# Kernel optimization log

Hardware: AMD Instinct MI355X
Metric: run time of the kernel (lower is better)

Reference implementation:

```python
import jax, jax.numpy as jnp
import numpy as np

NEG_INF = -1e38


def wkv(k, v, w, u):
    """Log-sum-exp-stabilized RWKV WKV scan.
    k, v: (B, T, C); w, u: (C,). Returns y: (B, T, C).
    """
    B, T, C = k.shape

    def step(carry, kv_t):
        num, den, mx = carry            # each (B, C)
        k_t, v_t = kv_t                 # (B, C)
        ku = k_t + u
        m = jnp.maximum(mx, ku)
        e1 = jnp.exp(mx - m)
        e2 = jnp.exp(ku - m)
        y = (e1 * num + e2 * v_t) / (e1 * den + e2)
        # state update
        mw = mx + w
        m2 = jnp.maximum(mw, k_t)
        es1 = jnp.exp(mw - m2)
        es2 = jnp.exp(k_t - m2)
        num = es1 * num + es2 * v_t
        den = es1 * den + es2
        return (num, den, m2), y

    init = (jnp.zeros((B, C), k.dtype),
            jnp.zeros((B, C), k.dtype),
            jnp.full((B, C), NEG_INF, k.dtype))
    _, y = jax.lax.scan(step, init, (jnp.swapaxes(k, 0, 1), jnp.swapaxes(v, 0, 1)))
    return jnp.swapaxes(y, 0, 1)


def setup_inputs() -> dict:
    key = jax.random.key(0)
    ks = jax.random.split(key, 8)
    B, T, C = 8, 4096, 512
    x = jax.random.normal(ks[0], (B, T, C), dtype=jnp.float32)
    # Linear weights stored as (in, out) so forward is x @ W.
    W_rkv = jax.random.normal(ks[1], (C, 6 * C), dtype=jnp.float32) / np.sqrt(C)
    W_out = jax.random.normal(ks[2], (2 * C, C), dtype=jnp.float32) / np.sqrt(2 * C)
    time_decay = jax.random.uniform(ks[3], (C,), minval=-6.0, maxval=-5.0, dtype=jnp.float32)
    time_first = jax.random.uniform(ks[4], (C,), minval=-3.0, maxval=0.0, dtype=jnp.float32)
    time_decay_rev = jax.random.uniform(ks[5], (C,), minval=-6.0, maxval=-5.0, dtype=jnp.float32)
    time_first_rev = jax.random.uniform(ks[6], (C,), minval=-3.0, maxval=0.0, dtype=jnp.float32)
    return {"x": x, "W_rkv": W_rkv, "W_out": W_out,
            "time_decay": time_decay, "time_first": time_first,
            "time_decay_rev": time_decay_rev, "time_first_rev": time_first_rev}


def reference(x, W_rkv, W_out, time_decay, time_first, time_decay_rev, time_first_rev):
    B, T, C = x.shape
    rkv = (x @ W_rkv).reshape(B, T, 2, 3, C)
    # forward direction
    r_f, k_f, v_f = rkv[:, :, 0, 0], rkv[:, :, 0, 1], rkv[:, :, 0, 2]
    w_f = -jnp.exp(time_decay)
    out_f = jax.nn.sigmoid(r_f) * wkv(k_f, v_f, w_f, time_first)
    # backward direction (run scan on time-reversed k/v, then reverse back)
    r_b, k_b, v_b = rkv[:, :, 1, 0], rkv[:, :, 1, 1], rkv[:, :, 1, 2]
    w_b = -jnp.exp(time_decay_rev)
    out_b = wkv(k_b[:, ::-1], v_b[:, ::-1], w_b, time_first_rev)[:, ::-1]
    out_b = jax.nn.sigmoid(r_b) * out_b
    out_cat = jnp.concatenate([out_f, out_b], axis=-1)  # (B, T, 2C)
    return out_cat @ W_out
```

## Files before the change

### kernel.cpp

```cpp
#include <hip/hip_runtime.h>

typedef float f4 __attribute__((ext_vector_type(4)));
typedef unsigned short us4 __attribute__((ext_vector_type(4)));
typedef unsigned short us8 __attribute__((ext_vector_type(8)));
typedef __bf16 bf16x8 __attribute__((ext_vector_type(8)));
typedef float f32x4 __attribute__((ext_vector_type(4)));
typedef _Float16 h8 __attribute__((ext_vector_type(8)));

#define TT 4096
#define CCH 512
#define NCH2 256
#define CHL2 16
#define NSEG 32
#define SEGC 8

__device__ __forceinline__ unsigned short f2bf(float f) {
  unsigned u = __builtin_bit_cast(unsigned, f);
  unsigned r = (u + 0x7FFFu + ((u >> 16) & 1u)) >> 16;
  return (unsigned short)r;
}
__device__ __forceinline__ void gload_lds16(const void* g, void* l) {
  __builtin_amdgcn_global_load_lds(
      (const __attribute__((address_space(1))) unsigned int*)g,
      (__attribute__((address_space(3))) unsigned int*)l, 16, 0, 0);
}
#define VMCNT(n) asm volatile("s_waitcnt vmcnt(" #n ")" ::: "memory")

__global__ __launch_bounds__(256)
void convert_f32_bf16(const float* __restrict__ in, unsigned short* __restrict__ out, int n4) {
  int i = blockIdx.x * 256 + threadIdx.x;
  if (i >= n4) return;
  f4 f = *(const f4*)(in + (size_t)i * 4);
  us4 o = { f2bf(f[0]), f2bf(f[1]), f2bf(f[2]), f2bf(f[3]) };
  *(us4*)(out + (size_t)i * 4) = o;
}

__global__ __launch_bounds__(256)
void transpose_to_bf16(const float* __restrict__ in, unsigned short* __restrict__ out,
                       int R, int Cc) {
  __shared__ unsigned short tile[32][33];
  int c0 = blockIdx.x * 32, r0 = blockIdx.y * 32;
  int tx = threadIdx.x, ty = threadIdx.y;
  #pragma unroll
  for (int j = 0; j < 32; j += 8)
    tile[ty + j][tx] = f2bf(in[(size_t)(r0 + ty + j) * Cc + c0 + tx]);
  __syncthreads();
  #pragma unroll
  for (int j = 0; j < 32; j += 8)
    out[(size_t)(c0 + ty + j) * R + r0 + tx] = tile[tx][ty + j];
}

__global__ __launch_bounds__(512, 2)
void gemm256_g1(const unsigned short* __restrict__ A,
                const unsigned short* __restrict__ BT,
                _Float16* __restrict__ kbuf, _Float16* __restrict__ vbuf,
                _Float16* __restrict__ rbuf) {
  __shared__ char lds[131072];
  const int tid = threadIdx.x;
  const int lane = tid & 63, wv = tid >> 6;
  const int wm = wv >> 2, wn = wv & 3;
  const int ln15 = lane & 15, lq = lane >> 4;

  const int nwg = gridDim.x;
  const int bid = blockIdx.x;
  const int wgid = (nwg % 8 == 0) ? (bid % 8) * (nwg / 8) + bid / 8 : bid;
  const int bn = wgid % 12, bm = wgid / 12;
  const size_t m0 = (size_t)bm * 256, n0 = (size_t)bn * 256;
  const char* Ab = (const char*)(A + m0 * 512);
  const char* Bb = (const char*)(BT + n0 * 512);

  const int srow0 = tid >> 2, srow1 = 128 + (tid >> 2);
  const int sg = tid & 3;
  const int sgs0 = (sg ^ ((srow0 >> 1) & 3)) << 4;
  const int sgs1 = (sg ^ ((srow1 >> 1) & 3)) << 4;

  auto STAGE = [&](int mat, int t, int h) {
    const char* gsrc = mat ? Bb : Ab;
    char* ldst = lds + mat * 65536 + ((t & 1) << 15) + (h << 14);
    const size_t co = (size_t)t * 128 + (size_t)h * 64;
    gload_lds16(gsrc + (size_t)srow0 * 1024 + co + sgs0, ldst + tid * 16);
    gload_lds16(gsrc + (size_t)srow1 * 1024 + co + sgs1, ldst + 8192 + tid * 16);
  };

  f32x4 acc[8][4] = {};
  STAGE(0, 0, 0); STAGE(1, 0, 0); STAGE(0, 0, 1); STAGE(1, 0, 1);

  for (int t = 0; t < 8; ++t) {
    char* Abase = lds + ((t & 1) << 15);
    char* Bbase = lds + 65536 + ((t & 1) << 15);
    VMCNT(4);
    __builtin_amdgcn_s_barrier();
    __builtin_amdgcn_sched_barrier(0);
    {
      bf16x8 bf[4], af[8];
      #pragma unroll
      for (int fn = 0; fn < 4; ++fn) {
        const int r = wn * 64 + fn * 16 + ln15;
        bf[fn] = *(const bf16x8*)(Bbase + r * 64 + ((lq ^ ((r >> 1) & 3)) << 4));
      }
      #pragma unroll
      for (int fm = 0; fm < 8; ++fm) {
        const int r = wm * 128 + fm * 16 + ln15;
        af[fm] = *(const bf16x8*)(Abase + r * 64 + ((lq ^ ((r >> 1) & 3)) << 4));
      }
      if (t < 7) { STAGE(0, t + 1, 0); STAGE(1, t + 1, 0); }
      __builtin_amdgcn_s_setprio(1);
      #pragma unroll
      for (int fm = 0; fm < 8; ++fm)
        #pragma unroll
        for (int fn = 0; fn < 4; ++fn)
          acc[fm][fn] = __builtin_amdgcn_mfma_f32_16x16x32_bf16(af[fm], bf[fn], acc[fm][fn], 0, 0, 0);
      __builtin_amdgcn_s_setprio(0);
    }
    if (t < 7) { VMCNT(4); } else { VMCNT(0); }
    __builtin_amdgcn_s_barrier();
    __builtin_amdgcn_sched_barrier(0);
    {
      bf16x8 bf[4], af[8];
      #pragma unroll
      for (int fn = 0; fn < 4; ++fn) {
        const int r = wn * 64 + fn * 16 + ln15;
        bf[fn] = *(const bf16x8*)(Bbase + 16384 + r * 64 + ((lq ^ ((r >> 1) & 3)) << 4));
      }
      #pragma unroll
      for (int fm = 0; fm < 8; ++fm) {
        const int r = wm * 128 + fm * 16 + ln15;
        af[fm] = *(const bf16x8*)(Abase + 16384 + r * 64 + ((lq ^ ((r >> 1) & 3)) << 4));
      }
      if (t < 7) { STAGE(0, t + 1, 1); STAGE(1, t + 1, 1); }
      __builtin_amdgcn_s_setprio(1);
      #pragma unroll
      for (int fm = 0; fm < 8; ++fm)
        #pragma unroll
        for (int fn = 0; fn < 4; ++fn)
          acc[fm][fn] = __builtin_amdgcn_mfma_f32_16x16x32_bf16(af[fm], bf[fn], acc[fm][fn], 0, 0, 0);
      __builtin_amdgcn_s_setprio(0);
    }
  }

  const int n0i = (int)n0;
  const int dir = (n0i >= 1536) ? 1 : 0;
  const int jj0 = n0i - dir * 1536;
  const int seg = jj0 >> 9;
  const int cbase = jj0 & 511;
  _Float16* dbuf = (seg == 0) ? rbuf : (seg == 1 ? kbuf : vbuf);
  float* stg = (float*)lds;
  const int ebnd = wv >> 2;
  const int erow = (tid >> 3) & 31;
  const int el8 = tid & 7;
  __syncthreads();
  #pragma unroll
  for (int gi = 0; gi < 4; ++gi) {
    #pragma unroll
    for (int f2 = 0; f2 < 2; ++f2) {
      const int fm = gi * 2 + f2;
      #pragma unroll
      for (int q = 0; q < 4; ++q) {
        const int rloc = f2 * 16 + lq * 4 + q;
        float* dst = stg + wm * 8192 + rloc * 256;
        const int sw = ((rloc >> 2) & 1) << 4;
        #pragma unroll
        for (int fn = 0; fn < 4; ++fn)
          dst[(wn * 64 + fn * 16 + ln15) ^ sw] = acc[fm][fn][q];
      }
    }
    __syncthreads();
    {
      const int rowg = (int)m0 + ebnd * 128 + gi * 32 + erow;
      const int b_ = rowg >> 12, tt = rowg & 4095;
      const int trow = dir ? (4095 - tt) : tt;
      _Float16* gp = dbuf + ((size_t)(b_ * 2 + dir) * TT + trow) * 512 + cbase;
      const float* sp = stg + ebnd * 8192 + erow * 256;
      const int sw = ((erow >> 2) & 1) << 4;
      #pragma unroll
      for (int u = 0; u < 4; ++u) {
        const int cf = el8 * 8 + u * 64;
        const int cs = cf ^ sw;
        f4 a = *(const f4*)(sp + cs);
        f4 b = *(const f4*)(sp + cs + 4);
        h8 hv = { (_Float16)a[0], (_Float16)a[1], (_Float16)a[2], (_Float16)a[3],
                  (_Float16)b[0], (_Float16)b[1], (_Float16)b[2], (_Float16)b[3] };
        *(h8*)(gp + cf) = hv;
      }
    }
    __syncthreads();
  }
}

__global__ __launch_bounds__(256)
void gemm_bf16_m1(const unsigned short* __restrict__ A, int lda,
                  const unsigned short* __restrict__ BT, int ldb,
                  int M, int N, int K, float* __restrict__ out) {
  __shared__ char smem[16384];
  unsigned short* As  = (unsigned short*)smem;
  unsigned short* Bsm = (unsigned short*)(smem + 8192);
  const int tid = threadIdx.x;
  const int lane = tid & 63, wv = tid >> 6;
  const int wr = wv >> 1, wc = wv & 1;
  const int ln15 = lane & 15, lq = lane >> 4;
  const int mtiles = M >> 7;
  const int bm = blockIdx.x % mtiles, bn = blockIdx.x / mtiles;
  const size_t m0 = (size_t)bm << 7, n0 = (size_t)bn << 7;
  f32x4 acc[4][4] = {};
  const char* Ab = (const char*)(A + m0 * (size_t)lda);
  const char* Bb = (const char*)(BT + n0 * (size_t)ldb);
  const int r0 = tid >> 2;
  const int cb = (((tid & 3) ^ (r0 & 3)) << 4);
  const size_t ldab = (size_t)lda * 2, ldbb = (size_t)ldb * 2;

  for (int k0 = 0; k0 < K; k0 += 32) {
    const size_t kb = (size_t)k0 * 2;
    gload_lds16(Ab + (size_t)r0 * ldab + kb + cb,        (char*)As + tid * 16);
    gload_lds16(Ab + (size_t)(r0 + 64) * ldab + kb + cb, (char*)As + 4096 + tid * 16);
    gload_lds16(Bb + (size_t)r0 * ldbb + kb + cb,        (char*)Bsm + tid * 16);
    gload_lds16(Bb + (size_t)(r0 + 64) * ldbb + kb + cb, (char*)Bsm + 4096 + tid * 16);
    __syncthreads();
    bf16x8 af[4], bg[4];
    #pragma unroll
    for (int i = 0; i < 4; ++i) {
      const int ar = wr * 64 + i * 16 + ln15;
      const int br = wc * 64 + i * 16 + ln15;
      af[i] = *(const bf16x8*)((char*)As  + ((ar * 4 + (lq ^ (ar & 3))) << 4));
      bg[i] = *(const bf16x8*)((char*)Bsm + ((br * 4 + (lq ^ (br & 3))) << 4));
    }
    #pragma unroll
    for (int i = 0; i < 4; ++i)
      #pragma unroll
      for (int j = 0; j < 4; ++j)
        acc[i][j] = __builtin_amdgcn_mfma_f32_16x16x32_bf16(af[i], bg[j], acc[i][j], 0, 0, 0);
    __syncthreads();
  }

  const int tq = tid >> 3, t8 = tid & 7;
  #pragma unroll
  for (int i = 0; i < 4; ++i) {
    __syncthreads();
    float* st = (float*)smem;
    #pragma unroll
    for (int j = 0; j < 4; ++j) {
      const int cl = wc * 64 + j * 16 + ln15;
      #pragma unroll
      for (int q = 0; q < 4; ++q) {
        const int rl = wr * 16 + lq * 4 + q;
        st[rl * 128 + (cl ^ (((rl >> 2) & 3) << 4))] = acc[i][j][q];
      }
    }
    __syncthreads();
    const int rl = tq, lqp = (rl >> 2) & 3;
    const int lr = ((rl >> 4) << 6) + (i << 4) + (rl & 15);
    const int rowg = (int)m0 + lr;
    #pragma unroll
    for (int u = 0; u < 4; ++u) {
      const int colL = t8 * 16 + u * 4;
      const int colS = colL ^ (lqp << 4);
      f4 vv = *(const f4*)(st + rl * 128 + colS);
      *(f4*)(out + (size_t)rowg * N + n0 + colL) = vv;
    }
  }
}

__global__ __launch_bounds__(128)
void wkv_pass1(const _Float16* __restrict__ kbuf, const _Float16* __restrict__ vbuf,
               const float* __restrict__ td, const float* __restrict__ tdr,
               float* __restrict__ cN, float* __restrict__ cD, float* __restrict__ cM) {
  const int bd = blockIdx.x;
  const int ch = blockIdx.y * 2 + threadIdx.y;
  const int dir = bd & 1;
  const int c = threadIdx.x * 8;
  const float* tdp = (dir ? tdr : td) + c;
  float w[8], num[8], den[8], m[8];
  #pragma unroll
  for (int e = 0; e < 8; ++e) { w[e] = -__expf(tdp[e]); num[e] = 0.f; den[e] = 0.f; m[e] = -1e38f; }
  const size_t base = ((size_t)bd * TT + (size_t)ch * CHL2) * CCH + c;
  const _Float16* kp = kbuf + base;
  const _Float16* vp = vbuf + base;
  h8 ka = *(const h8*)(kp), va = *(const h8*)(vp);
  h8 kb = *(const h8*)(kp + CCH), vb = *(const h8*)(vp + CCH);
  for (int t = 0; t < CHL2; ++t) {
    h8 kc = {}, vc = {};
    if (t + 2 < CHL2) {
      kc = *(const h8*)(kp + (size_t)(t + 2) * CCH);
      vc = *(const h8*)(vp + (size_t)(t + 2) * CCH);
    }
    #pragma unroll
    for (int e = 0; e < 8; ++e) {
      float ke = (float)ka[e], ve = (float)va[e];
      float mw = m[e] + w[e];
      float m2 = fmaxf(mw, ke);
      float e1 = __expf(mw - m2), e2 = __expf(ke - m2);
      num[e] = e1 * num[e] + e2 * ve;
      den[e] = e1 * den[e] + e2;
      m[e] = m2;
    }
    ka = kb; va = vb; kb = kc; vb = vc;
  }
  const size_t ci = ((size_t)bd * NCH2 + ch) * CCH + c;
  #pragma unroll
  for (int h = 0; h < 2; ++h) {
    *(f4*)(cN + ci + h * 4) = (f4){num[h*4], num[h*4+1], num[h*4+2], num[h*4+3]};
    *(f4*)(cD + ci + h * 4) = (f4){den[h*4], den[h*4+1], den[h*4+2], den[h*4+3]};
    *(f4*)(cM + ci + h * 4) = (f4){m[h*4], m[h*4+1], m[h*4+2], m[h*4+3]};
  }
}

__global__ __launch_bounds__(128)
void wkv_p2a(const float* __restrict__ td, const float* __restrict__ tdr,
             const float* __restrict__ cN, const float* __restrict__ cD,
             const float* __restrict__ cM,
             float* __restrict__ scN, float* __restrict__ scD, float* __restrict__ scM) {
  const int bd = blockIdx.x, seg = blockIdx.y;
  const int dir = bd & 1;
  const int c = threadIdx.x * 4;
  f4 tdv = *(const f4*)((dir ? tdr : td) + c);
  float dw[4], num[4], den[4], m[4];
  #pragma unroll
  for (int e = 0; e < 4; ++e) { dw[e] = -__expf(tdv[e]) * (float)CHL2; num[e] = 0.f; den[e] = 0.f; m[e] = -1e38f; }
  size_t ci = ((size_t)bd * NCH2 + (size_t)seg * SEGC) * CCH + c;
  for (int j = 0; j < SEGC; ++j, ci += CCH) {
    f4 ln = *(const f4*)(cN + ci);
    f4 ld = *(const f4*)(cD + ci);
    f4 lm = *(const f4*)(cM + ci);
    #pragma unroll
    for (int e = 0; e < 4; ++e) {
      float mp = m[e] + dw[e];
      float mm = fmaxf(mp, lm[e]);
      float e1 = __expf(mp - mm), e2 = __expf(lm[e] - mm);
      num[e] = e1 * num[e] + e2 * ln[e];
      den[e] = e1 * den[e] + e2 * ld[e];
      m[e] = mm;
    }
  }
  const size_t si = ((size_t)bd * NSEG + seg) * CCH + c;
  *(f4*)(scN + si) = (f4){num[0], num[1], num[2], num[3]};
  *(f4*)(scD + si) = (f4){den[0], den[1], den[2], den[3]};
  *(f4*)(scM + si) = (f4){m[0], m[1], m[2], m[3]};
}

__global__ __launch_bounds__(128)
void wkv_p2b(const float* __restrict__ td, const float* __restrict__ tdr,
             float* __restrict__ scN, float* __restrict__ scD, float* __restrict__ scM) {
  const int bd = blockIdx.x;
  const int dir = bd & 1;
  const int c = threadIdx.x * 4;
  f4 tdv = *(const f4*)((dir ? tdr : td) + c);
  float dws[4], num[4], den[4], m[4];
  #pragma unroll
  for (int e = 0; e < 4; ++e) { dws[e] = -__expf(tdv[e]) * (float)(CHL2 * SEGC); num[e] = 0.f; den[e] = 0.f; m[e] = -1e38f; }
  size_t si = (size_t)bd * NSEG * CCH + c;
  for (int s = 0; s < NSEG; ++s, si += CCH) {
    f4 ln = *(const f4*)(scN + si);
    f4 ld = *(const f4*)(scD + si);
    f4 lm = *(const f4*)(scM + si);
    *(f4*)(scN + si) = (f4){num[0], num[1], num[2], num[3]};
    *(f4*)(scD + si) = (f4){den[0], den[1], den[2], den[3]};
    *(f4*)(scM + si) = (f4){m[0], m[1], m[2], m[3]};
    #pragma unroll
    for (int e = 0; e < 4; ++e) {
      float mp = m[e] + dws[e];
      float mm = fmaxf(mp, lm[e]);
      float e1 = __expf(mp - mm), e2 = __expf(lm[e] - mm);
      num[e] = e1 * num[e] + e2 * ln[e];
      den[e] = e1 * den[e] + e2 * ld[e];
      m[e] = mm;
    }
  }
}

__global__ __launch_bounds__(128)
void wkv_p2c(const float* __restrict__ td, const float* __restrict__ tdr,
             const float* __restrict__ scN, const float* __restrict__ scD,
             const float* __restrict__ scM,
             float* __restrict__ cN, float* __restrict__ cD, float* __restrict__ cM) {
  const int bd = blockIdx.x, seg = blockIdx.y;
  const int dir = bd & 1;
  const int c = threadIdx.x * 4;
  f4 tdv = *(const f4*)((dir ? tdr : td) + c);
  const size_t si = ((size_t)bd * NSEG + seg) * CCH + c;
  f4 nv = *(const f4*)(scN + si);
  f4 dv = *(const f4*)(scD + si);
  f4 mv = *(const f4*)(scM + si);
  float dw[4], num[4], den[4], m[4];
  #pragma unroll
  for (int e = 0; e < 4; ++e) {
    dw[e] = -__expf(tdv[e]) * (float)CHL2;
    num[e] = nv[e]; den[e] = dv[e]; m[e] = mv[e];
  }
  size_t ci = ((size_t)bd * NCH2 + (size_t)seg * SEGC) * CCH + c;
  for (int j = 0; j < SEGC; ++j, ci += CCH) {
    f4 ln = *(const f4*)(cN + ci);
    f4 ld = *(const f4*)(cD + ci);
    f4 lm = *(const f4*)(cM + ci);
    *(f4*)(cN + ci) = (f4){num[0], num[1], num[2], num[3]};
    *(f4*)(cD + ci) = (f4){den[0], den[1], den[2], den[3]};
    *(f4*)(cM + ci) = (f4){m[0], m[1], m[2], m[3]};
    #pragma unroll
    for (int e = 0; e < 4; ++e) {
      float mp = m[e] + dw[e];
      float mm = fmaxf(mp, lm[e]);
      float e1 = __expf(mp - mm), e2 = __expf(lm[e] - mm);
      num[e] = e1 * num[e] + e2 * ln[e];
      den[e] = e1 * den[e] + e2 * ld[e];
      m[e] = mm;
    }
  }
}

__global__ __launch_bounds__(128)
void wkv_pass3(const _Float16* __restrict__ kbuf, const _Float16* __restrict__ vbuf,
               const _Float16* __restrict__ rbuf,
               const float* __restrict__ td, const float* __restrict__ tf,
               const float* __restrict__ tdr, const float* __restrict__ tfr,
               const float* __restrict__ cN, const float* __restrict__ cD,
               const float* __restrict__ cM,
               unsigned short* __restrict__ ocat) {
  const int bd = blockIdx.x;
  const int ch = blockIdx.y * 2 + threadIdx.y;
  const int b = bd >> 1, dir = bd & 1;
  const int c = threadIdx.x * 8;
  const float* tdp = (dir ? tdr : td) + c;
  const float* tup = (dir ? tfr : tf) + c;
  const size_t ci = ((size_t)bd * NCH2 + ch) * CCH + c;
  float w[8], u[8], num[8], den[8], m[8];
  #pragma unroll
  for (int e = 0; e < 8; ++e) {
    w[e] = -__expf(tdp[e]); u[e] = tup[e];
    num[e] = cN[ci + e]; den[e] = cD[ci + e]; m[e] = cM[ci + e];
  }
  const size_t base = ((size_t)bd * TT + (size_t)ch * CHL2) * CCH + c;
  const _Float16* kp = kbuf + base;
  const _Float16* vp = vbuf + base;
  const _Float16* rp = rbuf + base;
  h8 ka = *(const h8*)(kp), va = *(const h8*)(vp), ra = *(const h8*)(rp);
  h8 kb = *(const h8*)(kp + CCH), vb = *(const h8*)(vp + CCH), rb = *(const h8*)(rp + CCH);
  for (int t = 0; t < CHL2; ++t) {
    h8 kc = {}, vc = {}, rc = {};
    if (t + 2 < CHL2) {
      kc = *(const h8*)(kp + (size_t)(t + 2) * CCH);
      vc = *(const h8*)(vp + (size_t)(t + 2) * CCH);
      rc = *(const h8*)(rp + (size_t)(t + 2) * CCH);
    }
    const int tnat = ch * CHL2 + t;
    const int tact = dir ? (TT - 1 - tnat) : tnat;
    unsigned short o[8];
    #pragma unroll
    for (int e = 0; e < 8; ++e) {
      float ke = (float)ka[e], ve = (float)va[e];
      float ku = ke + u[e];
      float mm = fmaxf(m[e], ku);
      float e1 = __expf(m[e] - mm), e2 = __expf(ku - mm);
      float y = (e1 * num[e] + e2 * ve) * __builtin_amdgcn_rcpf(e1 * den[e] + e2);
      float rt = (float)ra[e];
      float sig = __builtin_amdgcn_rcpf(1.f + __expf(-rt));
      o[e] = f2bf(sig * y);
      float mw = m[e] + w[e];
      float m2 = fmaxf(mw, ke);
      float es1 = __expf(mw - m2), es2 = __expf(ke - m2);
      num[e] = es1 * num[e] + es2 * ve;
      den[e] = es1 * den[e] + es2;
      m[e] = m2;
    }
    us8 ov = { o[0], o[1], o[2], o[3], o[4], o[5], o[6], o[7] };
    *(us8*)(ocat + (((size_t)b * TT + tact) * 2 + dir) * CCH + c) = ov;
    ka = kb; va = vb; ra = rb; kb = kc; vb = vc; rb = rc;
  }
}

extern "C" void kernel_launch(void* const* d_in, const int* in_sizes, int n_in,
                              void* d_out, int out_size, void* d_ws, size_t ws_size,
                              hipStream_t stream) {
  const float* x   = (const float*)d_in[0];
  const float* Wr  = (const float*)d_in[1];
  const float* Wo  = (const float*)d_in[2];
  const float* td  = (const float*)d_in[3];
  const float* tf  = (const float*)d_in[4];
  const float* tdr = (const float*)d_in[5];
  const float* tfr = (const float*)d_in[6];
  float* out = (float*)d_out;

  auto rnd = [](size_t b) { return (b + 255) & ~(size_t)255; };
  const size_t wBytes = rnd((size_t)3072 * 512 * 2) + rnd((size_t)512 * 1024 * 2);
  auto need = [&](int Bs) {
    size_t s = wBytes;
    s += 3 * rnd((size_t)Bs * 2 * TT * 512 * 2);
    s += rnd((size_t)Bs * TT * 1024 * 2);
    s += 3 * rnd((size_t)Bs * 2 * (size_t)NCH2 * 512 * 4);
    s += 3 * rnd((size_t)Bs * 2 * (size_t)NSEG * 512 * 4);
    return s;
  };
  int Bs = 8;
  while (Bs > 1 && need(Bs) > ws_size) Bs >>= 1;

  char* ws = (char*)d_ws;
  size_t off = 0;
  auto alloc = [&](size_t bytes) -> char* {
    char* p = ws + off;
    off += (bytes + 255) & ~(size_t)255;
    return p;
  };
  unsigned short* wrkvT = (unsigned short*)alloc((size_t)3072 * 512 * 2);
  unsigned short* woutT = (unsigned short*)alloc((size_t)512 * 1024 * 2);
  _Float16*       kbuf  = (_Float16*)alloc((size_t)Bs * 2 * TT * 512 * 2);
  _Float16*       vbuf  = (_Float16*)alloc((size_t)Bs * 2 * TT * 512 * 2);
  _Float16*       rbuf  = (_Float16*)alloc((size_t)Bs * 2 * TT * 512 * 2);
  unsigned short* ocat  = (unsigned short*)alloc((size_t)Bs * TT * 1024 * 2);
  unsigned short* xb    = ocat;
  float*          cN    = (float*)alloc((size_t)Bs * 2 * (size_t)NCH2 * 512 * 4);
  float*          cD    = (float*)alloc((size_t)Bs * 2 * (size_t)NCH2 * 512 * 4);
  float*          cM    = (float*)alloc((size_t)Bs * 2 * (size_t)NCH2 * 512 * 4);
  float*          scN   = (float*)alloc((size_t)Bs * 2 * (size_t)NSEG * 512 * 4);
  float*          scD   = (float*)alloc((size_t)Bs * 2 * (size_t)NSEG * 512 * 4);
  float*          scM   = (float*)alloc((size_t)Bs * 2 * (size_t)NSEG * 512 * 4);

  transpose_to_bf16<<<dim3(3072 / 32, 512 / 32), dim3(32, 8), 0, stream>>>(Wr, wrkvT, 512, 3072);
  transpose_to_bf16<<<dim3(512 / 32, 1024 / 32), dim3(32, 8), 0, stream>>>(Wo, woutT, 1024, 512);

  const int nslices = 8 / Bs;
  const int Mslice = Bs * TT;
  const int mt256 = Mslice >> 8;
  const int mt128 = Mslice >> 7;
  for (int s = 0; s < nslices; ++s) {
    const float* xs = x + (size_t)s * Mslice * 512;
    float* outs = out + (size_t)s * Mslice * 512;
    convert_f32_bf16<<<Mslice * 512 / 1024, 256, 0, stream>>>(xs, xb, Mslice * 512 / 4);
    gemm256_g1<<<mt256 * 12, 512, 0, stream>>>(xb, wrkvT, kbuf, vbuf, rbuf);
    wkv_pass1<<<dim3(Bs * 2, NCH2 / 2), dim3(64, 2), 0, stream>>>(kbuf, vbuf, td, tdr, cN, cD, cM);
    wkv_p2a<<<dim3(Bs * 2, NSEG), 128, 0, stream>>>(td, tdr, cN, cD, cM, scN, scD, scM);
    wkv_p2b<<<Bs * 2, 128, 0, stream>>>(td, tdr, scN, scD, scM);
    wkv_p2c<<<dim3(Bs * 2, NSEG), 128, 0, stream>>>(td, tdr, scN, scD, scM, cN, cD, cM);
    wkv_pass3<<<dim3(Bs * 2, NCH2 / 2), dim3(64, 2), 0, stream>>>(kbuf, vbuf, rbuf, td, tf, tdr, tfr,
                                                                  cN, cD, cM, ocat);
    gemm_bf16_m1<<<mt128 * 4, 256, 0, stream>>>(ocat, 1024, woutT, 1024, Mslice, 512, 1024, outs);
  }
}
```

Baseline: 373.4 us.

## Write WKV output in place into rbuf and fold concat/reversal into output GEMM

```diff
diff --git a/kernel.cpp b/kernel.cpp
--- a/kernel.cpp
+++ b/kernel.cpp
@@ -2,7 +2,6 @@
 
 typedef float f4 __attribute__((ext_vector_type(4)));
 typedef unsigned short us4 __attribute__((ext_vector_type(4)));
-typedef unsigned short us8 __attribute__((ext_vector_type(8)));
 typedef __bf16 bf16x8 __attribute__((ext_vector_type(8)));
 typedef float f32x4 __attribute__((ext_vector_type(4)));
 typedef _Float16 h8 __attribute__((ext_vector_type(8)));
@@ -44,6 +43,21 @@
   #pragma unroll
   for (int j = 0; j < 32; j += 8)
     tile[ty + j][tx] = f2bf(in[(size_t)(r0 + ty + j) * Cc + c0 + tx]);
+  __syncthreads();
+  #pragma unroll
+  for (int j = 0; j < 32; j += 8)
+    out[(size_t)(c0 + ty + j) * R + r0 + tx] = tile[tx][ty + j];
+}
+
+__global__ __launch_bounds__(256)
+void transpose_to_f16(const float* __restrict__ in, _Float16* __restrict__ out,
+                      int R, int Cc) {
+  __shared__ _Float16 tile[32][33];
+  int c0 = blockIdx.x * 32, r0 = blockIdx.y * 32;
+  int tx = threadIdx.x, ty = threadIdx.y;
+  #pragma unroll
+  for (int j = 0; j < 32; j += 8)
+    tile[ty + j][tx] = (_Float16)in[(size_t)(r0 + ty + j) * Cc + c0 + tx];
   __syncthreads();
   #pragma unroll
   for (int j = 0; j < 32; j += 8)
@@ -188,12 +202,12 @@
 }
 
 __global__ __launch_bounds__(256)
-void gemm_bf16_m1(const unsigned short* __restrict__ A, int lda,
-                  const unsigned short* __restrict__ BT, int ldb,
-                  int M, int N, int K, float* __restrict__ out) {
+void gemm2_k(const _Float16* __restrict__ obuf,
+             const _Float16* __restrict__ BT,
+             int M, float* __restrict__ out) {
   __shared__ char smem[16384];
-  unsigned short* As  = (unsigned short*)smem;
-  unsigned short* Bsm = (unsigned short*)(smem + 8192);
+  _Float16* As  = (_Float16*)smem;
+  _Float16* Bsm = (_Float16*)(smem + 8192);
   const int tid = threadIdx.x;
   const int lane = tid & 63, wv = tid >> 6;
   const int wr = wv >> 1, wc = wv & 1;
@@ -202,32 +216,36 @@
   const int bm = blockIdx.x % mtiles, bn = blockIdx.x / mtiles;
   const size_t m0 = (size_t)bm << 7, n0 = (size_t)bn << 7;
   f32x4 acc[4][4] = {};
-  const char* Ab = (const char*)(A + m0 * (size_t)lda);
-  const char* Bb = (const char*)(BT + n0 * (size_t)ldb);
+  const int bB = (int)(m0 >> 12);
+  const int tbase = (int)(m0 & 4095);
+  const char* Bb = (const char*)(BT + n0 * 1024);
   const int r0 = tid >> 2;
   const int cb = (((tid & 3) ^ (r0 & 3)) << 4);
-  const size_t ldab = (size_t)lda * 2, ldbb = (size_t)ldb * 2;
-
-  for (int k0 = 0; k0 < K; k0 += 32) {
-    const size_t kb = (size_t)k0 * 2;
-    gload_lds16(Ab + (size_t)r0 * ldab + kb + cb,        (char*)As + tid * 16);
-    gload_lds16(Ab + (size_t)(r0 + 64) * ldab + kb + cb, (char*)As + 4096 + tid * 16);
-    gload_lds16(Bb + (size_t)r0 * ldbb + kb + cb,        (char*)Bsm + tid * 16);
-    gload_lds16(Bb + (size_t)(r0 + 64) * ldbb + kb + cb, (char*)Bsm + 4096 + tid * 16);
+
+  for (int k0 = 0; k0 < 1024; k0 += 32) {
+    const int half = k0 >> 9;
+    const size_t kb = (size_t)(k0 & 511) * 2;
+    const char* Ah = (const char*)(obuf + ((size_t)(bB * 2 + half) << 12) * 512);
+    const size_t ar0 = half ? (size_t)(4095 - (tbase + r0))      : (size_t)(tbase + r0);
+    const size_t ar1 = half ? (size_t)(4095 - (tbase + r0 + 64)) : (size_t)(tbase + r0 + 64);
+    gload_lds16(Ah + ar0 * 1024 + kb + cb, (char*)As + tid * 16);
+    gload_lds16(Ah + ar1 * 1024 + kb + cb, (char*)As + 4096 + tid * 16);
+    gload_lds16(Bb + (size_t)r0 * 2048 + (size_t)k0 * 2 + cb,        (char*)Bsm + tid * 16);
+    gload_lds16(Bb + (size_t)(r0 + 64) * 2048 + (size_t)k0 * 2 + cb, (char*)Bsm + 4096 + tid * 16);
     __syncthreads();
-    bf16x8 af[4], bg[4];
+    h8 af[4], bg[4];
     #pragma unroll
     for (int i = 0; i < 4; ++i) {
       const int ar = wr * 64 + i * 16 + ln15;
       const int br = wc * 64 + i * 16 + ln15;
-      af[i] = *(const bf16x8*)((char*)As  + ((ar * 4 + (lq ^ (ar & 3))) << 4));
-      bg[i] = *(const bf16x8*)((char*)Bsm + ((br * 4 + (lq ^ (br & 3))) << 4));
+      af[i] = *(const h8*)((char*)As  + ((ar * 4 + (lq ^ (ar & 3))) << 4));
+      bg[i] = *(const h8*)((char*)Bsm + ((br * 4 + (lq ^ (br & 3))) << 4));
     }
     #pragma unroll
     for (int i = 0; i < 4; ++i)
       #pragma unroll
       for (int j = 0; j < 4; ++j)
-        acc[i][j] = __builtin_amdgcn_mfma_f32_16x16x32_bf16(af[i], bg[j], acc[i][j], 0, 0, 0);
+        acc[i][j] = __builtin_amdgcn_mfma_f32_16x16x32_f16(af[i], bg[j], acc[i][j], 0, 0, 0);
     __syncthreads();
   }
 
@@ -254,7 +272,7 @@
       const int colL = t8 * 16 + u * 4;
       const int colS = colL ^ (lqp << 4);
       f4 vv = *(const f4*)(st + rl * 128 + colS);
-      *(f4*)(out + (size_t)rowg * N + n0 + colL) = vv;
+      *(f4*)(out + (size_t)rowg * 512 + n0 + colL) = vv;
     }
   }
 }
@@ -407,15 +425,14 @@
 
 __global__ __launch_bounds__(128)
 void wkv_pass3(const _Float16* __restrict__ kbuf, const _Float16* __restrict__ vbuf,
-               const _Float16* __restrict__ rbuf,
+               _Float16* __restrict__ rbuf,
                const float* __restrict__ td, const float* __restrict__ tf,
                const float* __restrict__ tdr, const float* __restrict__ tfr,
                const float* __restrict__ cN, const float* __restrict__ cD,
-               const float* __restrict__ cM,
-               unsigned short* __restrict__ ocat) {
+               const float* __restrict__ cM) {
   const int bd = blockIdx.x;
   const int ch = blockIdx.y * 2 + threadIdx.y;
-  const int b = bd >> 1, dir = bd & 1;
+  const int dir = bd & 1;
   const int c = threadIdx.x * 8;
   const float* tdp = (dir ? tdr : td) + c;
   const float* tup = (dir ? tfr : tf) + c;
@@ -429,7 +446,7 @@
   const size_t base = ((size_t)bd * TT + (size_t)ch * CHL2) * CCH + c;
   const _Float16* kp = kbuf + base;
   const _Float16* vp = vbuf + base;
-  const _Float16* rp = rbuf + base;
+  _Float16* rp = rbuf + base;
   h8 ka = *(const h8*)(kp), va = *(const h8*)(vp), ra = *(const h8*)(rp);
   h8 kb = *(const h8*)(kp + CCH), vb = *(const h8*)(vp + CCH), rb = *(const h8*)(rp + CCH);
   for (int t = 0; t < CHL2; ++t) {
@@ -439,9 +456,7 @@
       vc = *(const h8*)(vp + (size_t)(t + 2) * CCH);
       rc = *(const h8*)(rp + (size_t)(t + 2) * CCH);
     }
-    const int tnat = ch * CHL2 + t;
-    const int tact = dir ? (TT - 1 - tnat) : tnat;
-    unsigned short o[8];
+    _Float16 o[8];
     #pragma unroll
     for (int e = 0; e < 8; ++e) {
       float ke = (float)ka[e], ve = (float)va[e];
@@ -451,7 +466,7 @@
       float y = (e1 * num[e] + e2 * ve) * __builtin_amdgcn_rcpf(e1 * den[e] + e2);
       float rt = (float)ra[e];
       float sig = __builtin_amdgcn_rcpf(1.f + __expf(-rt));
-      o[e] = f2bf(sig * y);
+      o[e] = (_Float16)(sig * y);
       float mw = m[e] + w[e];
       float m2 = fmaxf(mw, ke);
       float es1 = __expf(mw - m2), es2 = __expf(ke - m2);
@@ -459,8 +474,8 @@
       den[e] = es1 * den[e] + es2;
       m[e] = m2;
     }
-    us8 ov = { o[0], o[1], o[2], o[3], o[4], o[5], o[6], o[7] };
-    *(us8*)(ocat + (((size_t)b * TT + tact) * 2 + dir) * CCH + c) = ov;
+    h8 ov = { o[0], o[1], o[2], o[3], o[4], o[5], o[6], o[7] };
+    *(h8*)(rp + (size_t)t * CCH) = ov;
     ka = kb; va = vb; ra = rb; kb = kc; vb = vc; rb = rc;
   }
 }
@@ -482,9 +497,7 @@
   auto need = [&](int Bs) {
     size_t s = wBytes;
     s += 3 * rnd((size_t)Bs * 2 * TT * 512 * 2);
-    s += rnd((size_t)Bs * TT * 1024 * 2);
-    s += 3 * rnd((size_t)Bs * 2 * (size_t)NCH2 * 512 * 4);
-    s += 3 * rnd((size_t)Bs * 2 * (size_t)NSEG * 512 * 4);
+    s += rnd((size_t)Bs * TT * 512 * 2);
     return s;
   };
   int Bs = 8;
@@ -498,21 +511,22 @@
     return p;
   };
   unsigned short* wrkvT = (unsigned short*)alloc((size_t)3072 * 512 * 2);
-  unsigned short* woutT = (unsigned short*)alloc((size_t)512 * 1024 * 2);
+  _Float16*       woutT = (_Float16*)alloc((size_t)512 * 1024 * 2);
   _Float16*       kbuf  = (_Float16*)alloc((size_t)Bs * 2 * TT * 512 * 2);
   _Float16*       vbuf  = (_Float16*)alloc((size_t)Bs * 2 * TT * 512 * 2);
   _Float16*       rbuf  = (_Float16*)alloc((size_t)Bs * 2 * TT * 512 * 2);
-  unsigned short* ocat  = (unsigned short*)alloc((size_t)Bs * TT * 1024 * 2);
-  unsigned short* xb    = ocat;
-  float*          cN    = (float*)alloc((size_t)Bs * 2 * (size_t)NCH2 * 512 * 4);
-  float*          cD    = (float*)alloc((size_t)Bs * 2 * (size_t)NCH2 * 512 * 4);
-  float*          cM    = (float*)alloc((size_t)Bs * 2 * (size_t)NCH2 * 512 * 4);
-  float*          scN   = (float*)alloc((size_t)Bs * 2 * (size_t)NSEG * 512 * 4);
-  float*          scD   = (float*)alloc((size_t)Bs * 2 * (size_t)NSEG * 512 * 4);
-  float*          scM   = (float*)alloc((size_t)Bs * 2 * (size_t)NSEG * 512 * 4);
+  unsigned short* xb    = (unsigned short*)alloc((size_t)Bs * TT * 512 * 2);
+  const size_t cs = (size_t)Bs * 2 * NCH2 * 512;
+  const size_t ss = (size_t)Bs * 2 * NSEG * 512;
+  float* cN  = (float*)xb;
+  float* cD  = cN + cs;
+  float* cM  = cD + cs;
+  float* scN = cM + cs;
+  float* scD = scN + ss;
+  float* scM = scD + ss;
 
   transpose_to_bf16<<<dim3(3072 / 32, 512 / 32), dim3(32, 8), 0, stream>>>(Wr, wrkvT, 512, 3072);
-  transpose_to_bf16<<<dim3(512 / 32, 1024 / 32), dim3(32, 8), 0, stream>>>(Wo, woutT, 1024, 512);
+  transpose_to_f16<<<dim3(512 / 32, 1024 / 32), dim3(32, 8), 0, stream>>>(Wo, woutT, 1024, 512);
 
   const int nslices = 8 / Bs;
   const int Mslice = Bs * TT;
@@ -528,7 +542,7 @@
     wkv_p2b<<<Bs * 2, 128, 0, stream>>>(td, tdr, scN, scD, scM);
     wkv_p2c<<<dim3(Bs * 2, NSEG), 128, 0, stream>>>(td, tdr, scN, scD, scM, cN, cD, cM);
     wkv_pass3<<<dim3(Bs * 2, NCH2 / 2), dim3(64, 2), 0, stream>>>(kbuf, vbuf, rbuf, td, tf, tdr, tfr,
-                                                                  cN, cD, cM, ocat);
-    gemm_bf16_m1<<<mt128 * 4, 256, 0, stream>>>(ocat, 1024, woutT, 1024, Mslice, 512, 1024, outs);
-  }
-}
+                                                                  cN, cD, cM);
+    gemm2_k<<<mt128 * 4, 256, 0, stream>>>(rbuf, woutT, Mslice, outs);
+  }
+}
```

After: 334.3 us. -10.5%, faster.
